# Optimization experiments

Measured on AMD Instinct MI355X. Metric: run time of the kernel, lower is better.

## Reference

```python
import jax, jax.numpy as jnp
import numpy as np

N = 100000   # nodes
E = 800000   # edges
L = 128      # latent_size
S = 15       # message passing steps
TW = 5       # time_window
OUT = 3      # output_size
NT = 3       # node types
NODE_F = 6   # 1+1+1+NT
EDGE_F = 7   # 2+1+2+1+1


def setup_inputs() -> dict:
    key = jax.random.key(0)
    ks = iter(jax.random.split(key, 80))
    def rn(shape, s=1.0):
        return jax.random.normal(next(ks), shape, jnp.float32) * s
    w = 0.05
    d = {}
    d["pvf"] = rn((N, 1))
    d["mat_param_D"] = rn((N, 1))
    d["mat_param_X"] = rn((N, 1))
    d["node_type"] = jax.random.randint(next(ks), (N,), 0, NT)
    d["mesh_pos"] = jax.random.uniform(next(ks), (N, 2), jnp.float32)
    d["world_pos"] = jax.random.uniform(next(ks), (N, 2), jnp.float32)
    d["senders"] = jax.random.randint(next(ks), (E,), 0, N)
    d["receivers"] = jax.random.randint(next(ks), (E,), 0, N)
    # normalizer stats
    d["node_norm_mean"] = rn((NODE_F,), 0.1); d["node_norm_std"] = jnp.ones((NODE_F,), jnp.float32)
    d["edge_norm_mean"] = rn((EDGE_F,), 0.1); d["edge_norm_std"] = jnp.ones((EDGE_F,), jnp.float32)
    # node encoder
    d["ne_w1"] = rn((NODE_F, L), w); d["ne_b1"] = jnp.zeros((L,), jnp.float32)
    d["ne_w2"] = rn((L, L), w);      d["ne_b2"] = jnp.zeros((L,), jnp.float32)
    d["ne_g"] = jnp.ones((L,), jnp.float32); d["ne_be"] = jnp.zeros((L,), jnp.float32)
    # edge encoder
    d["ee_w1"] = rn((EDGE_F, L), w); d["ee_b1"] = jnp.zeros((L,), jnp.float32)
    d["ee_w2"] = rn((L, L), w);      d["ee_b2"] = jnp.zeros((L,), jnp.float32)
    d["ee_g"] = jnp.ones((L,), jnp.float32); d["ee_be"] = jnp.zeros((L,), jnp.float32)
    # stacked GraphNetBlock params (S blocks)
    d["blk_ew1"] = rn((S, 3 * L, L), w); d["blk_eb1"] = jnp.zeros((S, L), jnp.float32)
    d["blk_ew2"] = rn((S, L, L), w);     d["blk_eb2"] = jnp.zeros((S, L), jnp.float32)
    d["blk_eg"] = jnp.ones((S, L), jnp.float32); d["blk_ebt"] = jnp.zeros((S, L), jnp.float32)
    d["blk_nw1"] = rn((S, 2 * L, L), w); d["blk_nb1"] = jnp.zeros((S, L), jnp.float32)
    d["blk_nw2"] = rn((S, L, L), w);     d["blk_nb2"] = jnp.zeros((S, L), jnp.float32)
    d["blk_ng"] = jnp.ones((S, L), jnp.float32); d["blk_nbt"] = jnp.zeros((S, L), jnp.float32)
    # decoder (Conv1d k=1 == per-node Linear)
    d["dec_w1"] = rn((L, 8), w); d["dec_b1"] = jnp.zeros((8,), jnp.float32)
    d["dec_w2"] = rn((8, OUT * TW), w); d["dec_b2"] = jnp.zeros((OUT * TW,), jnp.float32)
    return d


def _mlp_ln(x, w1, b1, w2, b2, g, b):
    # Linear-ReLU-Linear-ReLU-LayerNorm
    h = jax.nn.relu(x @ w1 + b1)
    h = jax.nn.relu(h @ w2 + b2)
    mu = jnp.mean(h, axis=-1, keepdims=True)
    var = jnp.var(h, axis=-1, keepdims=True)
    return (h - mu) * jax.lax.rsqrt(var + 1e-5) * g + b


def _forward(pvf, mat_param_D, mat_param_X, node_type, mesh_pos, world_pos, senders, receivers,
             node_norm_mean, node_norm_std, edge_norm_mean, edge_norm_std,
             ne_w1, ne_b1, ne_w2, ne_b2, ne_g, ne_be,
             ee_w1, ee_b1, ee_w2, ee_b2, ee_g, ee_be,
             blk_ew1, blk_eb1, blk_ew2, blk_eb2, blk_eg, blk_ebt,
             blk_nw1, blk_nb1, blk_nw2, blk_nb2, blk_ng, blk_nbt,
             dec_w1, dec_b1, dec_w2, dec_b2):
    # --- build features ---
    one_hot = jax.nn.one_hot(node_type, NT, dtype=jnp.float32)
    node_feats = jnp.concatenate([pvf, mat_param_D, mat_param_X, one_hot], axis=-1)   # [N, NODE_F]
    rel_m = mesh_pos[senders] - mesh_pos[receivers]
    dist_m = jnp.linalg.norm(rel_m, axis=-1, keepdims=True)
    rel_w = world_pos[senders] - world_pos[receivers]
    dist_w = jnp.linalg.norm(rel_w, axis=-1, keepdims=True)
    pvf_grad = pvf[senders] - pvf[receivers]
    edge_feats = jnp.concatenate([rel_m, dist_m, rel_w, dist_w, pvf_grad], axis=-1)   # [E, EDGE_F]
    # --- encode ---
    nl = _mlp_ln((node_feats - node_norm_mean) / node_norm_std, ne_w1, ne_b1, ne_w2, ne_b2, ne_g, ne_be)
    el = _mlp_ln((edge_feats - edge_norm_mean) / edge_norm_std, ee_w1, ee_b1, ee_w2, ee_b2, ee_g, ee_be)
    # --- process: S GraphNetBlocks with residuals ---
    def step(carry, p):
        nl, el = carry
        ew1, eb1, ew2, eb2, eg, ebt, nw1, nb1, nw2, nb2, ng, nbt = p
        edge_in = jnp.concatenate([nl[senders], nl[receivers], el], axis=-1)          # [E, 3L]
        new_e = _mlp_ln(edge_in, ew1, eb1, ew2, eb2, eg, ebt)
        aggr = jax.ops.segment_sum(new_e, receivers, num_segments=N)                  # [N, L]
        new_n = _mlp_ln(jnp.concatenate([nl, aggr], axis=-1), nw1, nb1, nw2, nb2, ng, nbt)
        return (nl + new_n, el + new_e), None
    (nl, el), _ = jax.lax.scan(step, (nl, el),
                               (blk_ew1, blk_eb1, blk_ew2, blk_eb2, blk_eg, blk_ebt,
                                blk_nw1, blk_nb1, blk_nw2, blk_nb2, blk_ng, blk_nbt))
    # --- decode (Conv1d k=1 == Linear) ---
    h = nl @ dec_w1 + dec_b1
    h = h * jax.nn.sigmoid(h)                                                         # Swish beta=1
    decoded = h @ dec_w2 + dec_b2                                                     # [N, OUT*TW]
    dt = jnp.repeat(jnp.arange(1, TW + 1, dtype=jnp.float32), OUT)                    # repeat_interleave
    delta = (decoded * dt).reshape(N, TW, OUT).transpose(1, 0, 2)                     # [TW, N, OUT]
    return delta


def reference(pvf, mat_param_D, mat_param_X, node_type, mesh_pos, world_pos, senders, receivers,
              node_norm_mean, node_norm_std, edge_norm_mean, edge_norm_std,
              ne_w1, ne_b1, ne_w2, ne_b2, ne_g, ne_be,
              ee_w1, ee_b1, ee_w2, ee_b2, ee_g, ee_be,
              blk_ew1, blk_eb1, blk_ew2, blk_eb2, blk_eg, blk_ebt,
              blk_nw1, blk_nb1, blk_nw2, blk_nb2, blk_ng, blk_nbt,
              dec_w1, dec_b1, dec_w2, dec_b2):
    return _forward(pvf, mat_param_D, mat_param_X, node_type, mesh_pos, world_pos, senders, receivers,
                    node_norm_mean, node_norm_std, edge_norm_mean, edge_norm_std,
                    ne_w1, ne_b1, ne_w2, ne_b2, ne_g, ne_be,
                    ee_w1, ee_b1, ee_w2, ee_b2, ee_g, ee_be,
                    blk_ew1, blk_eb1, blk_ew2, blk_eb2, blk_eg, blk_ebt,
                    blk_nw1, blk_nb1, blk_nw2, blk_nb2, blk_ng, blk_nbt,
                    dec_w1, dec_b1, dec_w2, dec_b2)
```

## Files before the change

kernel.cpp:

```cpp
#include <hip/hip_runtime.h>
#include <math.h>

#define NNODES 100000
#define NEDGES 800000
#define L 128
#define NBSCAN ((NNODES + 255) / 256)

typedef unsigned short u16;
typedef unsigned int u32;
typedef unsigned short ushort8 __attribute__((ext_vector_type(8)));
typedef _Float16 f16x8 __attribute__((ext_vector_type(8)));
typedef __attribute__((ext_vector_type(4))) float f32x4;

static __device__ __forceinline__ float h2f(u16 u) {
    _Float16 h;
    __builtin_memcpy(&h, &u, 2);
    return (float)h;
}
static __device__ __forceinline__ u16 f2h(float x) {
    _Float16 h = (_Float16)x;
    u16 u;
    __builtin_memcpy(&u, &h, 2);
    return u;
}
static __device__ __forceinline__ void load8h(const u16* p, float* d) {
    ushort8 v = *(const ushort8*)p;
    #pragma unroll
    for (int k = 0; k < 8; k++) d[k] = h2f(v[k]);
}
static __device__ __forceinline__ void atomic_pk_add_f16(u16* addr, u32 data) {
    asm volatile("global_atomic_pk_add_f16 %0, %1, off" :: "v"(addr), "v"(data));
}

__global__ __launch_bounds__(256) void zero_kernel(uint4* p, int n) {
    int i = blockIdx.x * 256 + threadIdx.x;
    if (i < n) p[i] = make_uint4(0u, 0u, 0u, 0u);
}

__global__ __launch_bounds__(256) void diag_kernel(float* out, int n, float val) {
    int i = blockIdx.x * 256 + threadIdx.x;
    if (i < n) out[i] = val;
}

__global__ __launch_bounds__(256) void count_kernel(
    const int* __restrict__ receivers, u32* __restrict__ counts)
{
    int e = blockIdx.x * 256 + threadIdx.x;
    if (e < NEDGES) atomicAdd(&counts[receivers[e]], 1u);
}

__global__ __launch_bounds__(256) void scan_block_kernel(
    const u32* __restrict__ counts, u32* __restrict__ offsets,
    u32* __restrict__ partials)
{
    __shared__ u32 sh[256];
    int i = blockIdx.x * 256 + threadIdx.x;
    u32 c = (i < NNODES) ? counts[i] : 0u;
    sh[threadIdx.x] = c;
    __syncthreads();
    #pragma unroll
    for (int d = 1; d < 256; d <<= 1) {
        u32 v = (threadIdx.x >= d) ? sh[threadIdx.x - d] : 0u;
        __syncthreads();
        sh[threadIdx.x] += v;
        __syncthreads();
    }
    if (i < NNODES) offsets[i] = sh[threadIdx.x] - c;
    if (threadIdx.x == 255) partials[blockIdx.x] = sh[255];
}

__global__ __launch_bounds__(512) void scan_partials_kernel(u32* __restrict__ partials)
{
    __shared__ u32 sh[512];
    int x = threadIdx.x;
    u32 c = (x < NBSCAN) ? partials[x] : 0u;
    sh[x] = c;
    __syncthreads();
    #pragma unroll
    for (int d = 1; d < 512; d <<= 1) {
        u32 v = (x >= d) ? sh[x - d] : 0u;
        __syncthreads();
        sh[x] += v;
        __syncthreads();
    }
    if (x < NBSCAN) partials[x] = sh[x] - c;
}

__global__ __launch_bounds__(256) void add_offsets_kernel(
    u32* __restrict__ offsets, const u32* __restrict__ partials,
    u32* __restrict__ cursor)
{
    int i = blockIdx.x * 256 + threadIdx.x;
    if (i < NNODES) {
        u32 v = offsets[i] + partials[blockIdx.x];
        offsets[i] = v;
        cursor[i] = v;
    }
}

__global__ __launch_bounds__(256) void scatter_kernel(
    const int* __restrict__ senders, const int* __restrict__ receivers,
    u32* __restrict__ cursor, int* __restrict__ ssorted, int* __restrict__ rsorted)
{
    int e = blockIdx.x * 256 + threadIdx.x;
    if (e < NEDGES) {
        int r = receivers[e];
        u32 pos = atomicAdd(&cursor[r], 1u);
        ssorted[pos] = senders[e];
        rsorted[pos] = r;
    }
}

__global__ __launch_bounds__(256) void pack_weights_kernel(
    const float* __restrict__ src, u16* __restrict__ dst, int K, int nsteps)
{
    int idx = blockIdx.x * 256 + threadIdx.x;
    int nkk = K >> 5;
    int total = nsteps * 8 * nkk * 64;
    if (idx >= total) return;
    int lane = idx & 63;
    int rest = idx >> 6;
    int kk = rest % nkk; rest /= nkk;
    int nb = rest & 7;
    int s = rest >> 3;
    int c15 = lane & 15, gg = lane >> 4;
    const float* w = src + (size_t)s * K * 128;
    u16 out[8];
    #pragma unroll
    for (int j = 0; j < 8; j++) {
        int k = kk * 32 + gg * 8 + j;
        out[j] = f2h(w[(size_t)k * 128 + nb * 16 + c15]);
    }
    *(ushort8*)(dst + (size_t)idx * 8) = *(ushort8*)out;
}

__global__ __launch_bounds__(256) void pack_ee1_kernel(
    const float* __restrict__ src, u16* __restrict__ dst)
{
    int idx = blockIdx.x * 256 + threadIdx.x;
    if (idx >= 8 * 64) return;
    int lane = idx & 63, nb = idx >> 6;
    int c15 = lane & 15, gg = lane >> 4;
    u16 out[8];
    #pragma unroll
    for (int j = 0; j < 8; j++) {
        int k = gg * 8 + j;
        out[j] = (k < 7) ? f2h(src[(size_t)k * 128 + nb * 16 + c15]) : (u16)0;
    }
    *(ushort8*)(dst + (size_t)idx * 8) = *(ushort8*)out;
}

__global__ __launch_bounds__(256) void node_encode_kernel(
    const float* __restrict__ pvf, const float* __restrict__ matD,
    const float* __restrict__ matX, const int* __restrict__ ntype,
    const float* __restrict__ nmean, const float* __restrict__ nstd,
    const float* __restrict__ w1, const float* __restrict__ b1,
    const float* __restrict__ w2, const float* __restrict__ b2,
    const float* __restrict__ g, const float* __restrict__ be,
    u16* __restrict__ nl)
{
    __shared__ float xs[64][8];
    __shared__ float h[64][132];
    const int t = threadIdx.x;
    const int base = blockIdx.x * 64;
    if (t < 64) {
        int n = base + t;
        if (n < NNODES) {
            int nt = ntype[n];
            float f[6];
            f[0] = pvf[n]; f[1] = matD[n]; f[2] = matX[n];
            f[3] = (nt == 0) ? 1.f : 0.f;
            f[4] = (nt == 1) ? 1.f : 0.f;
            f[5] = (nt == 2) ? 1.f : 0.f;
            #pragma unroll
            for (int k = 0; k < 6; k++) xs[t][k] = (f[k] - nmean[k]) / nstd[k];
        } else {
            #pragma unroll
            for (int k = 0; k < 6; k++) xs[t][k] = 0.f;
        }
    }
    __syncthreads();
    const int j = t & 127, half = t >> 7;
    for (int i = 0; i < 32; i++) {
        int e = half * 32 + i;
        float acc = b1[j];
        #pragma unroll
        for (int k = 0; k < 6; k++) acc += xs[e][k] * w1[k * L + j];
        h[e][j] = fmaxf(acc, 0.f);
    }
    __syncthreads();
    float acc2[32];
    #pragma unroll
    for (int i = 0; i < 32; i++) acc2[i] = b2[j];
    for (int k4 = 0; k4 < 32; k4++) {
        const float* wp = w2 + k4 * 4 * L + j;
        float wa = wp[0], wb = wp[L], wc = wp[2 * L], wd = wp[3 * L];
        #pragma unroll
        for (int i = 0; i < 32; i++) {
            const float4 xv = *(const float4*)&h[half * 32 + i][k4 * 4];
            acc2[i] += xv.x * wa + xv.y * wb + xv.z * wc + xv.w * wd;
        }
    }
    __syncthreads();
    #pragma unroll
    for (int i = 0; i < 32; i++) h[half * 32 + i][j] = fmaxf(acc2[i], 0.f);
    __syncthreads();
    {
        const int e = t >> 2, tg = t & 3;
        float sum = 0.f, sq = 0.f;
        #pragma unroll
        for (int jj = 0; jj < 32; jj++) { float v = h[e][tg * 32 + jj]; sum += v; sq += v * v; }
        sum += __shfl_xor(sum, 1); sq += __shfl_xor(sq, 1);
        sum += __shfl_xor(sum, 2); sq += __shfl_xor(sq, 2);
        float mu = sum * (1.f / 128.f);
        float rstd = rsqrtf(sq * (1.f / 128.f) - mu * mu + 1e-5f);
        int n = base + e;
        if (n < NNODES) {
            u32* nrow = (u32*)(nl + (size_t)n * L) + tg * 16;
            #pragma unroll
            for (int p = 0; p < 16; p++) {
                int f0 = tg * 32 + 2 * p;
                float v0 = (h[e][f0] - mu) * rstd * g[f0] + be[f0];
                float v1 = (h[e][f0 + 1] - mu) * rstd * g[f0 + 1] + be[f0 + 1];
                nrow[p] = (u32)f2h(v0) | ((u32)f2h(v1) << 16);
            }
        }
    }
}

__global__ __launch_bounds__(256, 2) void edge_encode_kernel(
    const int* __restrict__ ssorted, const int* __restrict__ rsorted,
    const float* __restrict__ pvf, const float* __restrict__ mesh,
    const float* __restrict__ world,
    const float* __restrict__ emean, const float* __restrict__ estd,
    const u16* __restrict__ wp1, const float* __restrict__ b1,
    const u16* __restrict__ wp2, const float* __restrict__ b2,
    const float* __restrict__ gamma, const float* __restrict__ beta,
    u16* __restrict__ el)
{
    __shared__ __align__(16) u16 hbuf[4][2][4][64][8];
    const int t = threadIdx.x;
    const int wid = t >> 6, lane = t & 63;
    const int c15 = lane & 15, g = lane >> 4;
    const int base = blockIdx.x * 256 + wid * 64;

    f16x8 a[4];
    #pragma unroll
    for (int m = 0; m < 4; m++) {
        f16x8 v;
        #pragma unroll
        for (int k = 0; k < 8; k++) v[k] = (_Float16)0.f;
        if (g == 0) {
            int e = base + m * 16 + c15;
            int s = ssorted[e], r = rsorted[e];
            float rmx = mesh[s * 2] - mesh[r * 2];
            float rmy = mesh[s * 2 + 1] - mesh[r * 2 + 1];
            float dm = sqrtf(rmx * rmx + rmy * rmy);
            float rwx = world[s * 2] - world[r * 2];
            float rwy = world[s * 2 + 1] - world[r * 2 + 1];
            float dw = sqrtf(rwx * rwx + rwy * rwy);
            float pg = pvf[s] - pvf[r];
            float f[7] = {rmx, rmy, dm, rwx, rwy, dw, pg};
            #pragma unroll
            for (int k = 0; k < 7; k++)
                v[k] = (_Float16)((f[k] - emean[k]) / estd[k]);
        }
        a[m] = v;
    }

    f32x4 acc[8][4];
    #pragma unroll
    for (int nb = 0; nb < 8; nb++) {
        float bv = b1[nb * 16 + c15];
        #pragma unroll
        for (int m = 0; m < 4; m++) acc[nb][m] = (f32x4){bv, bv, bv, bv};
    }
    #pragma unroll
    for (int nb = 0; nb < 8; nb++) {
        f16x8 b = *(const f16x8*)(wp1 + ((size_t)(nb * 64 + lane)) * 8);
        #pragma unroll
        for (int m = 0; m < 4; m++)
            acc[nb][m] = __builtin_amdgcn_mfma_f32_16x16x32_f16(a[m], b, acc[nb][m], 0, 0, 0);
    }

    float gamv[8], btv[8];
    #pragma unroll
    for (int nb = 0; nb < 8; nb++) {
        gamv[nb] = gamma[nb * 16 + c15];
        btv[nb] = beta[nb * 16 + c15];
    }
    #pragma unroll
    for (int mp = 0; mp < 2; mp++) {
        #pragma unroll
        for (int ml = 0; ml < 2; ml++) {
            int m = mp * 2 + ml;
            #pragma unroll
            for (int nb = 0; nb < 8; nb++) {
                int kk2 = nb >> 1;
                int sub = ((nb & 1) << 1) | (c15 >> 3);
                int jj = c15 & 7;
                #pragma unroll
                for (int i = 0; i < 4; i++) {
                    float v = fmaxf(acc[nb][m][i], 0.f);
                    hbuf[wid][ml][kk2][g * 4 + i + 16 * sub][jj] = f2h(v);
                }
            }
        }
        f32x4 acc2[2][8];
        #pragma unroll
        for (int nb = 0; nb < 8; nb++) {
            float bv = b2[nb * 16 + c15];
            acc2[0][nb] = (f32x4){bv, bv, bv, bv};
            acc2[1][nb] = (f32x4){bv, bv, bv, bv};
        }
        #pragma unroll
        for (int kk = 0; kk < 4; kk++) {
            f16x8 a0 = *(const f16x8*)&hbuf[wid][0][kk][lane][0];
            f16x8 a1 = *(const f16x8*)&hbuf[wid][1][kk][lane][0];
            #pragma unroll
            for (int nb = 0; nb < 8; nb++) {
                f16x8 b = *(const f16x8*)(wp2 + ((size_t)(nb * 4 + kk) * 64 + lane) * 8);
                acc2[0][nb] = __builtin_amdgcn_mfma_f32_16x16x32_f16(a0, b, acc2[0][nb], 0, 0, 0);
                acc2[1][nb] = __builtin_amdgcn_mfma_f32_16x16x32_f16(a1, b, acc2[1][nb], 0, 0, 0);
            }
        }
        #pragma unroll
        for (int ml = 0; ml < 2; ml++) {
            float muv[4], rsv[4];
            #pragma unroll
            for (int i = 0; i < 4; i++) {
                float p = 0.f, q = 0.f;
                #pragma unroll
                for (int nb = 0; nb < 8; nb++) {
                    float v = fmaxf(acc2[ml][nb][i], 0.f);
                    acc2[ml][nb][i] = v;
                    p += v; q += v * v;
                }
                p += __shfl_xor(p, 1); q += __shfl_xor(q, 1);
                p += __shfl_xor(p, 2); q += __shfl_xor(q, 2);
                p += __shfl_xor(p, 4); q += __shfl_xor(q, 4);
                p += __shfl_xor(p, 8); q += __shfl_xor(q, 8);
                float mu = p * (1.f / 128.f);
                muv[i] = mu;
                rsv[i] = rsqrtf(q * (1.f / 128.f) - mu * mu + 1e-5f);
            }
            #pragma unroll
            for (int i = 0; i < 4; i++) {
                int erow = base + (mp * 2 + ml) * 16 + g * 4 + i;
                #pragma unroll
                for (int nb = 0; nb < 8; nb++) {
                    float v = (acc2[ml][nb][i] - muv[i]) * rsv[i] * gamv[nb] + btv[nb];
                    float pv = __shfl_xor(v, 1);
                    if (!(c15 & 1)) {
                        *(u32*)(el + (size_t)erow * L + nb * 16 + c15) =
                            (u32)f2h(v) | ((u32)f2h(pv) << 16);
                    }
                }
            }
        }
    }
}

#define EDGE_LOAD_A(nk, slot)                                                     \
    {                                                                             \
        _Pragma("unroll")                                                         \
        for (int m = 0; m < 4; m++) {                                             \
            const u16* ap;                                                        \
            if ((nk) < 4)      ap = nl + (size_t)sA[m] * L + (nk) * 32 + g * 8;   \
            else if ((nk) < 8) ap = nl + (size_t)rA[m] * L + ((nk) - 4) * 32 + g * 8; \
            else               ap = el + (size_t)(base + m * 16 + c15) * L + ((nk) - 8) * 32 + g * 8; \
            ab[slot][m] = *(const f16x8*)ap;                                      \
        }                                                                         \
    }

#define NODE_LOAD_A(nk, slot)                                                     \
    {                                                                             \
        _Pragma("unroll")                                                         \
        for (int m = 0; m < 4; m++) {                                             \
            const u16* ap = ((nk) < 4) ? (nl + (size_t)rowL[m] * L + (nk) * 32 + g * 8) \
                                       : (aggr + (size_t)rowL[m] * L + ((nk) - 4) * 32 + g * 8); \
            ab[slot][m] = *(const f16x8*)ap;                                      \
        }                                                                         \
    }

#define LGKM_BARRIER()                                          \
    asm volatile("s_waitcnt lgkmcnt(0)" ::: "memory");          \
    __builtin_amdgcn_sched_barrier(0);                          \
    __builtin_amdgcn_s_barrier();

__global__ __launch_bounds__(256, 2) void edge_block_kernel(
    const int* __restrict__ ssorted, const int* __restrict__ rsorted,
    const u16* __restrict__ nl, u16* __restrict__ el, u16* __restrict__ aggr,
    const u16* __restrict__ wp1, const float* __restrict__ b1,
    const u16* __restrict__ wp2, const float* __restrict__ b2,
    const float* __restrict__ gamma, const float* __restrict__ beta)
{
    __shared__ __align__(16) u16 wbuf[2][8][64][8];
    __shared__ __align__(16) u16 hbuf[4][2][4][64][8];
    const int t = threadIdx.x;
    const int wid = t >> 6, lane = t & 63;
    const int c15 = lane & 15, g = lane >> 4;
    const int base = blockIdx.x * 256 + wid * 64;

    int sA[4], rA[4];
    #pragma unroll
    for (int m = 0; m < 4; m++) {
        sA[m] = ssorted[base + m * 16 + c15];
        rA[m] = rsorted[base + m * 16 + c15];
    }

    f32x4 acc[8][4];
    #pragma unroll
    for (int nb = 0; nb < 8; nb++) {
        float bv = b1[nb * 16 + c15];
        #pragma unroll
        for (int m = 0; m < 4; m++) acc[nb][m] = (f32x4){bv, bv, bv, bv};
    }
    f16x8 ab[2][4];
    f16x8 w0, w1;
    w0 = *(const f16x8*)(wp1 + ((size_t)((2 * wid) * 12 + 0) * 64 + lane) * 8);
    w1 = *(const f16x8*)(wp1 + ((size_t)((2 * wid + 1) * 12 + 0) * 64 + lane) * 8);
    EDGE_LOAD_A(0, 0);
    *(f16x8*)&wbuf[0][2 * wid][lane][0] = w0;
    *(f16x8*)&wbuf[0][2 * wid + 1][lane][0] = w1;
    LGKM_BARRIER();

    #pragma unroll
    for (int kk = 0; kk < 12; kk++) {
        if (kk < 11) {
            w0 = *(const f16x8*)(wp1 + ((size_t)((2 * wid) * 12 + kk + 1) * 64 + lane) * 8);
            w1 = *(const f16x8*)(wp1 + ((size_t)((2 * wid + 1) * 12 + kk + 1) * 64 + lane) * 8);
            EDGE_LOAD_A(kk + 1, (kk + 1) & 1);
        }
        __builtin_amdgcn_s_setprio(1);
        #pragma unroll
        for (int nb = 0; nb < 8; nb++) {
            f16x8 b = *(const f16x8*)&wbuf[kk & 1][nb][lane][0];
            #pragma unroll
            for (int m = 0; m < 4; m++)
                acc[nb][m] = __builtin_amdgcn_mfma_f32_16x16x32_f16(ab[kk & 1][m], b, acc[nb][m], 0, 0, 0);
        }
        __builtin_amdgcn_s_setprio(0);
        if (kk < 11) {
            *(f16x8*)&wbuf[(kk + 1) & 1][2 * wid][lane][0] = w0;
            *(f16x8*)&wbuf[(kk + 1) & 1][2 * wid + 1][lane][0] = w1;
            LGKM_BARRIER();
        }
    }

    float gamv[8], btv[8];
    #pragma unroll
    for (int nb = 0; nb < 8; nb++) {
        gamv[nb] = gamma[nb * 16 + c15];
        btv[nb] = beta[nb * 16 + c15];
    }
    #pragma unroll
    for (int mp = 0; mp < 2; mp++) {
        #pragma unroll
        for (int ml = 0; ml < 2; ml++) {
            int m = mp * 2 + ml;
            #pragma unroll
            for (int nb = 0; nb < 8; nb++) {
                int kk2 = nb >> 1;
                int sub = ((nb & 1) << 1) | (c15 >> 3);
                int jj = c15 & 7;
                #pragma unroll
                for (int i = 0; i < 4; i++) {
                    float v = fmaxf(acc[nb][m][i], 0.f);
                    hbuf[wid][ml][kk2][g * 4 + i + 16 * sub][jj] = f2h(v);
                }
            }
        }
        f32x4 acc2[2][8];
        #pragma unroll
        for (int nb = 0; nb < 8; nb++) {
            float bv = b2[nb * 16 + c15];
            acc2[0][nb] = (f32x4){bv, bv, bv, bv};
            acc2[1][nb] = (f32x4){bv, bv, bv, bv};
        }
        __builtin_amdgcn_s_setprio(1);
        #pragma unroll
        for (int kk = 0; kk < 4; kk++) {
            f16x8 a0 = *(const f16x8*)&hbuf[wid][0][kk][lane][0];
            f16x8 a1 = *(const f16x8*)&hbuf[wid][1][kk][lane][0];
            #pragma unroll
            for (int nb = 0; nb < 8; nb++) {
                f16x8 b = *(const f16x8*)(wp2 + ((size_t)(nb * 4 + kk) * 64 + lane) * 8);
                acc2[0][nb] = __builtin_amdgcn_mfma_f32_16x16x32_f16(a0, b, acc2[0][nb], 0, 0, 0);
                acc2[1][nb] = __builtin_amdgcn_mfma_f32_16x16x32_f16(a1, b, acc2[1][nb], 0, 0, 0);
            }
        }
        __builtin_amdgcn_s_setprio(0);
        #pragma unroll
        for (int ml = 0; ml < 2; ml++) {
            const int slot = mp * 2 + ml;
            float muv[4], rsv[4];
            #pragma unroll
            for (int i = 0; i < 4; i++) {
                float p = 0.f, q = 0.f;
                #pragma unroll
                for (int nb = 0; nb < 8; nb++) {
                    float v = fmaxf(acc2[ml][nb][i], 0.f);
                    acc2[ml][nb][i] = v;
                    p += v; q += v * v;
                }
                p += __shfl_xor(p, 1); q += __shfl_xor(q, 1);
                p += __shfl_xor(p, 2); q += __shfl_xor(q, 2);
                p += __shfl_xor(p, 4); q += __shfl_xor(q, 4);
                p += __shfl_xor(p, 8); q += __shfl_xor(q, 8);
                float mu = p * (1.f / 128.f);
                muv[i] = mu;
                rsv[i] = rsqrtf(q * (1.f / 128.f) - mu * mu + 1e-5f);
            }
            float av[8], apv[8];
            #pragma unroll
            for (int nb = 0; nb < 8; nb++) { av[nb] = 0.f; apv[nb] = 0.f; }
            int cur = rsorted[base + slot * 16 + g * 4];
            #pragma unroll
            for (int i = 0; i < 4; i++) {
                int erow = base + slot * 16 + g * 4 + i;
                int ri = (i == 0) ? cur : rsorted[erow];
                float vv[8], pp[8];
                #pragma unroll
                for (int nb = 0; nb < 8; nb++) {
                    float v = (acc2[ml][nb][i] - muv[i]) * rsv[i] * gamv[nb] + btv[nb];
                    vv[nb] = v;
                    pp[nb] = __shfl_xor(v, 1);
                }
                u32 olds[8];
                if (!(c15 & 1)) {
                    #pragma unroll
                    for (int nb = 0; nb < 8; nb++)
                        olds[nb] = *(const u32*)(el + (size_t)erow * L + nb * 16 + c15);
                }
                if (ri != cur) {
                    #pragma unroll
                    for (int nb = 0; nb < 8; nb++) {
                        if (!(c15 & 1)) {
                            u32 add = (u32)f2h(av[nb]) | ((u32)f2h(apv[nb]) << 16);
                            atomic_pk_add_f16(aggr + (size_t)cur * L + nb * 16 + c15, add);
                        }
                        av[nb] = 0.f; apv[nb] = 0.f;
                    }
                    cur = ri;
                }
                #pragma unroll
                for (int nb = 0; nb < 8; nb++) {
                    av[nb] += vv[nb];
                    apv[nb] += pp[nb];
                    if (!(c15 & 1)) {
                        float r0 = h2f((u16)(olds[nb] & 0xFFFFu)) + vv[nb];
                        float r1 = h2f((u16)(olds[nb] >> 16)) + pp[nb];
                        *(u32*)(el + (size_t)erow * L + nb * 16 + c15) =
                            (u32)f2h(r0) | ((u32)f2h(r1) << 16);
                    }
                }
            }
            #pragma unroll
            for (int nb = 0; nb < 8; nb++) {
                if (!(c15 & 1)) {
                    u32 add = (u32)f2h(av[nb]) | ((u32)f2h(apv[nb]) << 16);
                    atomic_pk_add_f16(aggr + (size_t)cur * L + nb * 16 + c15, add);
                }
            }
        }
    }
}

__global__ __launch_bounds__(256, 2) void node_block_kernel(
    u16* __restrict__ nl, u16* __restrict__ aggr,
    const u16* __restrict__ wp1, const float* __restrict__ b1,
    const u16* __restrict__ wp2, const float* __restrict__ b2,
    const float* __restrict__ gamma, const float* __restrict__ beta)
{
    __shared__ __align__(16) u16 wbuf[2][8][64][8];
    __shared__ __align__(16) u16 hbuf[4][2][4][64][8];
    const int t = threadIdx.x;
    const int wid = t >> 6, lane = t & 63;
    const int c15 = lane & 15, g = lane >> 4;
    const int base = blockIdx.x * 256 + wid * 64;

    int rowL[4];
    #pragma unroll
    for (int m = 0; m < 4; m++) {
        int r = base + m * 16 + c15;
        rowL[m] = r < NNODES ? r : 0;
    }

    f32x4 acc[8][4];
    #pragma unroll
    for (int nb = 0; nb < 8; nb++) {
        float bv = b1[nb * 16 + c15];
        #pragma unroll
        for (int m = 0; m < 4; m++) acc[nb][m] = (f32x4){bv, bv, bv, bv};
    }
    f16x8 ab[2][4];
    f16x8 w0, w1;
    w0 = *(const f16x8*)(wp1 + ((size_t)((2 * wid) * 8 + 0) * 64 + lane) * 8);
    w1 = *(const f16x8*)(wp1 + ((size_t)((2 * wid + 1) * 8 + 0) * 64 + lane) * 8);
    NODE_LOAD_A(0, 0);
    *(f16x8*)&wbuf[0][2 * wid][lane][0] = w0;
    *(f16x8*)&wbuf[0][2 * wid + 1][lane][0] = w1;
    LGKM_BARRIER();

    #pragma unroll
    for (int kk = 0; kk < 8; kk++) {
        if (kk < 7) {
            w0 = *(const f16x8*)(wp1 + ((size_t)((2 * wid) * 8 + kk + 1) * 64 + lane) * 8);
            w1 = *(const f16x8*)(wp1 + ((size_t)((2 * wid + 1) * 8 + kk + 1) * 64 + lane) * 8);
            NODE_LOAD_A(kk + 1, (kk + 1) & 1);
        }
        __builtin_amdgcn_s_setprio(1);
        #pragma unroll
        for (int nb = 0; nb < 8; nb++) {
            f16x8 b = *(const f16x8*)&wbuf[kk & 1][nb][lane][0];
            #pragma unroll
            for (int m = 0; m < 4; m++)
                acc[nb][m] = __builtin_amdgcn_mfma_f32_16x16x32_f16(ab[kk & 1][m], b, acc[nb][m], 0, 0, 0);
        }
        __builtin_amdgcn_s_setprio(0);
        if (kk < 7) {
            *(f16x8*)&wbuf[(kk + 1) & 1][2 * wid][lane][0] = w0;
            *(f16x8*)&wbuf[(kk + 1) & 1][2 * wid + 1][lane][0] = w1;
            LGKM_BARRIER();
        }
    }

    {
        const uint4 z4 = make_uint4(0u, 0u, 0u, 0u);
        #pragma unroll
        for (int m = 0; m < 4; m++) {
            int r = base + m * 16 + c15;
            if (r < NNODES) {
                #pragma unroll
                for (int kk = 0; kk < 4; kk++)
                    *(uint4*)(aggr + (size_t)r * L + kk * 32 + g * 8) = z4;
            }
        }
    }

    float gamv[8], btv[8];
    #pragma unroll
    for (int nb = 0; nb < 8; nb++) {
        gamv[nb] = gamma[nb * 16 + c15];
        btv[nb] = beta[nb * 16 + c15];
    }
    #pragma unroll
    for (int mp = 0; mp < 2; mp++) {
        #pragma unroll
        for (int ml = 0; ml < 2; ml++) {
            int m = mp * 2 + ml;
            #pragma unroll
            for (int nb = 0; nb < 8; nb++) {
                int kk2 = nb >> 1;
                int sub = ((nb & 1) << 1) | (c15 >> 3);
                int jj = c15 & 7;
                #pragma unroll
                for (int i = 0; i < 4; i++) {
                    float v = fmaxf(acc[nb][m][i], 0.f);
                    hbuf[wid][ml][kk2][g * 4 + i + 16 * sub][jj] = f2h(v);
                }
            }
        }
        f32x4 acc2[2][8];
        #pragma unroll
        for (int nb = 0; nb < 8; nb++) {
            float bv = b2[nb * 16 + c15];
            acc2[0][nb] = (f32x4){bv, bv, bv, bv};
            acc2[1][nb] = (f32x4){bv, bv, bv, bv};
        }
        __builtin_amdgcn_s_setprio(1);
        #pragma unroll
        for (int kk = 0; kk < 4; kk++) {
            f16x8 a0 = *(const f16x8*)&hbuf[wid][0][kk][lane][0];
            f16x8 a1 = *(const f16x8*)&hbuf[wid][1][kk][lane][0];
            #pragma unroll
            for (int nb = 0; nb < 8; nb++) {
                f16x8 b = *(const f16x8*)(wp2 + ((size_t)(nb * 4 + kk) * 64 + lane) * 8);
                acc2[0][nb] = __builtin_amdgcn_mfma_f32_16x16x32_f16(a0, b, acc2[0][nb], 0, 0, 0);
                acc2[1][nb] = __builtin_amdgcn_mfma_f32_16x16x32_f16(a1, b, acc2[1][nb], 0, 0, 0);
            }
        }
        __builtin_amdgcn_s_setprio(0);
        #pragma unroll
        for (int ml = 0; ml < 2; ml++) {
            float muv[4], rsv[4];
            #pragma unroll
            for (int i = 0; i < 4; i++) {
                float p = 0.f, q = 0.f;
                #pragma unroll
                for (int nb = 0; nb < 8; nb++) {
                    float v = fmaxf(acc2[ml][nb][i], 0.f);
                    acc2[ml][nb][i] = v;
                    p += v; q += v * v;
                }
                p += __shfl_xor(p, 1); q += __shfl_xor(q, 1);
                p += __shfl_xor(p, 2); q += __shfl_xor(q, 2);
                p += __shfl_xor(p, 4); q += __shfl_xor(q, 4);
                p += __shfl_xor(p, 8); q += __shfl_xor(q, 8);
                float mu = p * (1.f / 128.f);
                muv[i] = mu;
                rsv[i] = rsqrtf(q * (1.f / 128.f) - mu * mu + 1e-5f);
            }
            #pragma unroll
            for (int i = 0; i < 4; i++) {
                int nrow = base + (mp * 2 + ml) * 16 + g * 4 + i;
                #pragma unroll
                for (int nb = 0; nb < 8; nb++) {
                    float v = (acc2[ml][nb][i] - muv[i]) * rsv[i] * gamv[nb] + btv[nb];
                    float pv = __shfl_xor(v, 1);
                    if (!(c15 & 1) && nrow < NNODES) {
                        int col = nb * 16 + c15;
                        u32* nlp = (u32*)(nl + (size_t)nrow * L + col);
                        u32 old = *nlp;
                        float r0 = h2f((u16)(old & 0xFFFFu)) + v;
                        float r1 = h2f((u16)(old >> 16)) + pv;
                        *nlp = (u32)f2h(r0) | ((u32)f2h(r1) << 16);
                    }
                }
            }
        }
    }
}

__global__ __launch_bounds__(256) void decode_kernel(
    const u16* __restrict__ nl,
    const float* __restrict__ w1, const float* __restrict__ b1,
    const float* __restrict__ w2, const float* __restrict__ b2,
    float* __restrict__ out)
{
    int n = blockIdx.x * blockDim.x + threadIdx.x;
    if (n >= NNODES) return;
    float h8[8];
    #pragma unroll
    for (int jj = 0; jj < 8; jj++) h8[jj] = b1[jj];
    const u16* row = nl + (size_t)n * L;
    for (int k = 0; k < L; k += 8) {
        float xv[8];
        load8h(row + k, xv);
        #pragma unroll
        for (int q = 0; q < 8; q++)
            #pragma unroll
            for (int jj = 0; jj < 8; jj++)
                h8[jj] += xv[q] * w1[(k + q) * 8 + jj];
    }
    #pragma unroll
    for (int jj = 0; jj < 8; jj++) { float v = h8[jj]; h8[jj] = v / (1.f + expf(-v)); }
    #pragma unroll
    for (int o15 = 0; o15 < 15; o15++) {
        float accv = b2[o15];
        #pragma unroll
        for (int jj = 0; jj < 8; jj++) accv += h8[jj] * w2[jj * 15 + o15];
        int tt = o15 / 3, oo = o15 - tt * 3;
        out[(size_t)tt * NNODES * 3 + (size_t)n * 3 + oo] = accv * (float)(tt + 1);
    }
}

extern "C" void kernel_launch(void* const* d_in, const int* in_sizes, int n_in,
                              void* d_out, int out_size, void* d_ws, size_t ws_size,
                              hipStream_t stream)
{
    const size_t AG_B = (size_t)NNODES * L * 2;
    const size_t EL_B = (size_t)NEDGES * L * 2;
    const size_t NL_B = (size_t)NNODES * L * 2;
    const size_t PE1_N = (size_t)15 * 8 * 12 * 64 * 8;
    const size_t PE2_N = (size_t)15 * 8 * 4 * 64 * 8;
    const size_t PN1_N = (size_t)15 * 8 * 8 * 64 * 8;
    const size_t PN2_N = (size_t)15 * 8 * 4 * 64 * 8;
    const size_t PEE1_N = (size_t)8 * 64 * 8;
    const size_t PEE2_N = (size_t)8 * 4 * 64 * 8;
    const size_t WPK_B = (PE1_N + PE2_N + PN1_N + PN2_N + PEE1_N + PEE2_N) * 2;
    const size_t SS_B  = (size_t)NEDGES * 4;
    const size_t RS_B  = (size_t)NEDGES * 4;
    const size_t CNT_B = (size_t)NNODES * 4;
    const size_t OFF_B = (size_t)NNODES * 4;
    const size_t CUR_B = (size_t)NNODES * 4;
    const size_t PAR_B = 2048;
    const size_t TOTAL = AG_B + EL_B + NL_B + WPK_B + SS_B + RS_B
                       + CNT_B + OFF_B + CUR_B + PAR_B;

    if (ws_size < TOTAL) {
        float val = 1000.0f + (float)((double)ws_size * 1e-6);
        diag_kernel<<<(out_size + 255) / 256, 256, 0, stream>>>((float*)d_out, out_size, val);
        return;
    }

    char* wsp = (char*)d_ws;
    u16* aggr = (u16*)wsp;                 wsp += AG_B;
    u16* el   = (u16*)wsp;                 wsp += EL_B;
    u16* nl   = (u16*)wsp;                 wsp += NL_B;
    u16* pe1  = (u16*)wsp;                 wsp += PE1_N * 2;
    u16* pe2  = (u16*)wsp;                 wsp += PE2_N * 2;
    u16* pn1  = (u16*)wsp;                 wsp += PN1_N * 2;
    u16* pn2  = (u16*)wsp;                 wsp += PN2_N * 2;
    u16* pee1 = (u16*)wsp;                 wsp += PEE1_N * 2;
    u16* pee2 = (u16*)wsp;                 wsp += PEE2_N * 2;
    int* ssorted = (int*)wsp;              wsp += SS_B;
    int* rsorted = (int*)wsp;              wsp += RS_B;
    u32* counts  = (u32*)wsp;              wsp += CNT_B;
    u32* offsets = (u32*)wsp;              wsp += OFF_B;
    u32* cursor  = (u32*)wsp;              wsp += CUR_B;
    u32* partials = (u32*)wsp;             wsp += PAR_B;
    float* out = (float*)d_out;

    const float* pvf       = (const float*)d_in[0];
    const float* matD      = (const float*)d_in[1];
    const float* matX      = (const float*)d_in[2];
    const int*   ntype     = (const int*)d_in[3];
    const float* mesh      = (const float*)d_in[4];
    const float* world     = (const float*)d_in[5];
    const int*   senders   = (const int*)d_in[6];
    const int*   receivers = (const int*)d_in[7];
    const float* nmean = (const float*)d_in[8];
    const float* nstd  = (const float*)d_in[9];
    const float* emean = (const float*)d_in[10];
    const float* estd  = (const float*)d_in[11];
    const float* ne_w1 = (const float*)d_in[12];
    const float* ne_b1 = (const float*)d_in[13];
    const float* ne_w2 = (const float*)d_in[14];
    const float* ne_b2 = (const float*)d_in[15];
    const float* ne_g  = (const float*)d_in[16];
    const float* ne_be = (const float*)d_in[17];
    const float* ee_w1 = (const float*)d_in[18];
    const float* ee_b1 = (const float*)d_in[19];
    const float* ee_w2 = (const float*)d_in[20];
    const float* ee_b2 = (const float*)d_in[21];
    const float* ee_g  = (const float*)d_in[22];
    const float* ee_be = (const float*)d_in[23];
    const float* blk_ew1 = (const float*)d_in[24];
    const float* blk_eb1 = (const float*)d_in[25];
    const float* blk_ew2 = (const float*)d_in[26];
    const float* blk_eb2 = (const float*)d_in[27];
    const float* blk_eg  = (const float*)d_in[28];
    const float* blk_ebt = (const float*)d_in[29];
    const float* blk_nw1 = (const float*)d_in[30];
    const float* blk_nb1 = (const float*)d_in[31];
    const float* blk_nw2 = (const float*)d_in[32];
    const float* blk_nb2 = (const float*)d_in[33];
    const float* blk_ng  = (const float*)d_in[34];
    const float* blk_nbt = (const float*)d_in[35];
    const float* dec_w1 = (const float*)d_in[36];
    const float* dec_b1 = (const float*)d_in[37];
    const float* dec_w2 = (const float*)d_in[38];
    const float* dec_b2 = (const float*)d_in[39];

    zero_kernel<<<(int)((CNT_B / 16 + 255) / 256), 256, 0, stream>>>((uint4*)counts, (int)(CNT_B / 16));
    count_kernel<<<(NEDGES + 255) / 256, 256, 0, stream>>>(receivers, counts);
    scan_block_kernel<<<NBSCAN, 256, 0, stream>>>(counts, offsets, partials);
    scan_partials_kernel<<<1, 512, 0, stream>>>(partials);
    add_offsets_kernel<<<NBSCAN, 256, 0, stream>>>(offsets, partials, cursor);
    scatter_kernel<<<(NEDGES + 255) / 256, 256, 0, stream>>>(senders, receivers, cursor, ssorted, rsorted);

    pack_weights_kernel<<<(int)((15 * 8 * 12 * 64 + 255) / 256), 256, 0, stream>>>(
        blk_ew1, pe1, 384, 15);
    pack_weights_kernel<<<(int)((15 * 8 * 4 * 64 + 255) / 256), 256, 0, stream>>>(
        blk_ew2, pe2, 128, 15);
    pack_weights_kernel<<<(int)((15 * 8 * 8 * 64 + 255) / 256), 256, 0, stream>>>(
        blk_nw1, pn1, 256, 15);
    pack_weights_kernel<<<(int)((15 * 8 * 4 * 64 + 255) / 256), 256, 0, stream>>>(
        blk_nw2, pn2, 128, 15);
    pack_ee1_kernel<<<2, 256, 0, stream>>>(ee_w1, pee1);
    pack_weights_kernel<<<(int)((8 * 4 * 64 + 255) / 256), 256, 0, stream>>>(
        ee_w2, pee2, 128, 1);

    node_encode_kernel<<<(NNODES + 63) / 64, 256, 0, stream>>>(
        pvf, matD, matX, ntype, nmean, nstd,
        ne_w1, ne_b1, ne_w2, ne_b2, ne_g, ne_be, nl);
    edge_encode_kernel<<<NEDGES / 256, 256, 0, stream>>>(
        ssorted, rsorted, pvf, mesh, world, emean, estd,
        pee1, ee_b1, pee2, ee_b2, ee_g, ee_be, el);

    const int nzero = NNODES * L * 2 / 16;
    zero_kernel<<<(nzero + 255) / 256, 256, 0, stream>>>((uint4*)aggr, nzero);

    for (int s = 0; s < 15; s++) {
        edge_block_kernel<<<NEDGES / 256, 256, 0, stream>>>(
            ssorted, rsorted, nl, el, aggr,
            pe1 + (size_t)s * 8 * 12 * 64 * 8, blk_eb1 + s * L,
            pe2 + (size_t)s * 8 * 4 * 64 * 8,  blk_eb2 + s * L,
            blk_eg + s * L, blk_ebt + s * L);
        node_block_kernel<<<(NNODES + 255) / 256, 256, 0, stream>>>(
            nl, aggr,
            pn1 + (size_t)s * 8 * 8 * 64 * 8, blk_nb1 + s * L,
            pn2 + (size_t)s * 8 * 4 * 64 * 8, blk_nb2 + s * L,
            blk_ng + s * L, blk_nbt + s * L);
    }

    decode_kernel<<<(NNODES + 255) / 256, 256, 0, stream>>>(
        nl, dec_w1, dec_b1, dec_w2, dec_b2, out);
}
```

Before: 6.844 ms.

## Use single-wave blocks with per-wave register weight prefetch instead of shared LDS tiles

```diff
diff --git a/kernel.cpp b/kernel.cpp
--- a/kernel.cpp
+++ b/kernel.cpp
@@ -383,24 +383,21 @@
         }                                                                         \
     }
 
-#define LGKM_BARRIER()                                          \
+#define WAVE_LDS_FENCE()                                        \
     asm volatile("s_waitcnt lgkmcnt(0)" ::: "memory");          \
-    __builtin_amdgcn_sched_barrier(0);                          \
-    __builtin_amdgcn_s_barrier();
-
-__global__ __launch_bounds__(256, 2) void edge_block_kernel(
+    __builtin_amdgcn_sched_barrier(0);
+
+__global__ __launch_bounds__(64, 2) void edge_block_kernel(
     const int* __restrict__ ssorted, const int* __restrict__ rsorted,
     const u16* __restrict__ nl, u16* __restrict__ el, u16* __restrict__ aggr,
     const u16* __restrict__ wp1, const float* __restrict__ b1,
     const u16* __restrict__ wp2, const float* __restrict__ b2,
     const float* __restrict__ gamma, const float* __restrict__ beta)
 {
-    __shared__ __align__(16) u16 wbuf[2][8][64][8];
-    __shared__ __align__(16) u16 hbuf[4][2][4][64][8];
-    const int t = threadIdx.x;
-    const int wid = t >> 6, lane = t & 63;
+    __shared__ __align__(16) u16 hbuf[2][4][64][8];
+    const int lane = threadIdx.x & 63;
     const int c15 = lane & 15, g = lane >> 4;
-    const int base = blockIdx.x * 256 + wid * 64;
+    const int base = blockIdx.x * 64;
 
     int sA[4], rA[4];
     #pragma unroll
@@ -417,35 +414,30 @@
         for (int m = 0; m < 4; m++) acc[nb][m] = (f32x4){bv, bv, bv, bv};
     }
     f16x8 ab[2][4];
-    f16x8 w0, w1;
-    w0 = *(const f16x8*)(wp1 + ((size_t)((2 * wid) * 12 + 0) * 64 + lane) * 8);
-    w1 = *(const f16x8*)(wp1 + ((size_t)((2 * wid + 1) * 12 + 0) * 64 + lane) * 8);
+    f16x8 bbuf[2][8];
+    #pragma unroll
+    for (int nb = 0; nb < 8; nb++)
+        bbuf[0][nb] = *(const f16x8*)(wp1 + ((size_t)(nb * 12) * 64 + lane) * 8);
     EDGE_LOAD_A(0, 0);
-    *(f16x8*)&wbuf[0][2 * wid][lane][0] = w0;
-    *(f16x8*)&wbuf[0][2 * wid + 1][lane][0] = w1;
-    LGKM_BARRIER();
 
     #pragma unroll
     for (int kk = 0; kk < 12; kk++) {
         if (kk < 11) {
-            w0 = *(const f16x8*)(wp1 + ((size_t)((2 * wid) * 12 + kk + 1) * 64 + lane) * 8);
-            w1 = *(const f16x8*)(wp1 + ((size_t)((2 * wid + 1) * 12 + kk + 1) * 64 + lane) * 8);
+            #pragma unroll
+            for (int nb = 0; nb < 8; nb++)
+                bbuf[(kk + 1) & 1][nb] =
+                    *(const f16x8*)(wp1 + ((size_t)(nb * 12 + kk + 1) * 64 + lane) * 8);
             EDGE_LOAD_A(kk + 1, (kk + 1) & 1);
         }
         __builtin_amdgcn_s_setprio(1);
         #pragma unroll
         for (int nb = 0; nb < 8; nb++) {
-            f16x8 b = *(const f16x8*)&wbuf[kk & 1][nb][lane][0];
             #pragma unroll
             for (int m = 0; m < 4; m++)
-                acc[nb][m] = __builtin_amdgcn_mfma_f32_16x16x32_f16(ab[kk & 1][m], b, acc[nb][m], 0, 0, 0);
+                acc[nb][m] = __builtin_amdgcn_mfma_f32_16x16x32_f16(
+                    ab[kk & 1][m], bbuf[kk & 1][nb], acc[nb][m], 0, 0, 0);
         }
         __builtin_amdgcn_s_setprio(0);
-        if (kk < 11) {
-            *(f16x8*)&wbuf[(kk + 1) & 1][2 * wid][lane][0] = w0;
-            *(f16x8*)&wbuf[(kk + 1) & 1][2 * wid + 1][lane][0] = w1;
-            LGKM_BARRIER();
-        }
     }
 
     float gamv[8], btv[8];
@@ -467,10 +459,11 @@
                 #pragma unroll
                 for (int i = 0; i < 4; i++) {
                     float v = fmaxf(acc[nb][m][i], 0.f);
-                    hbuf[wid][ml][kk2][g * 4 + i + 16 * sub][jj] = f2h(v);
-                }
-            }
-        }
+                    hbuf[ml][kk2][g * 4 + i + 16 * sub][jj] = f2h(v);
+                }
+            }
+        }
+        WAVE_LDS_FENCE();
         f32x4 acc2[2][8];
         #pragma unroll
         for (int nb = 0; nb < 8; nb++) {
@@ -481,8 +474,8 @@
         __builtin_amdgcn_s_setprio(1);
         #pragma unroll
         for (int kk = 0; kk < 4; kk++) {
-            f16x8 a0 = *(const f16x8*)&hbuf[wid][0][kk][lane][0];
-            f16x8 a1 = *(const f16x8*)&hbuf[wid][1][kk][lane][0];
+            f16x8 a0 = *(const f16x8*)&hbuf[0][kk][lane][0];
+            f16x8 a1 = *(const f16x8*)&hbuf[1][kk][lane][0];
             #pragma unroll
             for (int nb = 0; nb < 8; nb++) {
                 f16x8 b = *(const f16x8*)(wp2 + ((size_t)(nb * 4 + kk) * 64 + lane) * 8);
@@ -491,6 +484,7 @@
             }
         }
         __builtin_amdgcn_s_setprio(0);
+        WAVE_LDS_FENCE();
         #pragma unroll
         for (int ml = 0; ml < 2; ml++) {
             const int slot = mp * 2 + ml;
@@ -567,18 +561,16 @@
     }
 }
 
-__global__ __launch_bounds__(256, 2) void node_block_kernel(
+__global__ __launch_bounds__(64, 2) void node_block_kernel(
     u16* __restrict__ nl, u16* __restrict__ aggr,
     const u16* __restrict__ wp1, const float* __restrict__ b1,
     const u16* __restrict__ wp2, const float* __restrict__ b2,
     const float* __restrict__ gamma, const float* __restrict__ beta)
 {
-    __shared__ __align__(16) u16 wbuf[2][8][64][8];
-    __shared__ __align__(16) u16 hbuf[4][2][4][64][8];
-    const int t = threadIdx.x;
-    const int wid = t >> 6, lane = t & 63;
+    __shared__ __align__(16) u16 hbuf[2][4][64][8];
+    const int lane = threadIdx.x & 63;
     const int c15 = lane & 15, g = lane >> 4;
-    const int base = blockIdx.x * 256 + wid * 64;
+    const int base = blockIdx.x * 64;
 
     int rowL[4];
     #pragma unroll
@@ -595,35 +587,30 @@
         for (int m = 0; m < 4; m++) acc[nb][m] = (f32x4){bv, bv, bv, bv};
     }
     f16x8 ab[2][4];
-    f16x8 w0, w1;
-    w0 = *(const f16x8*)(wp1 + ((size_t)((2 * wid) * 8 + 0) * 64 + lane) * 8);
-    w1 = *(const f16x8*)(wp1 + ((size_t)((2 * wid + 1) * 8 + 0) * 64 + lane) * 8);
+    f16x8 bbuf[2][8];
+    #pragma unroll
+    for (int nb = 0; nb < 8; nb++)
+        bbuf[0][nb] = *(const f16x8*)(wp1 + ((size_t)(nb * 8) * 64 + lane) * 8);
     NODE_LOAD_A(0, 0);
-    *(f16x8*)&wbuf[0][2 * wid][lane][0] = w0;
-    *(f16x8*)&wbuf[0][2 * wid + 1][lane][0] = w1;
-    LGKM_BARRIER();
 
     #pragma unroll
     for (int kk = 0; kk < 8; kk++) {
         if (kk < 7) {
-            w0 = *(const f16x8*)(wp1 + ((size_t)((2 * wid) * 8 + kk + 1) * 64 + lane) * 8);
-            w1 = *(const f16x8*)(wp1 + ((size_t)((2 * wid + 1) * 8 + kk + 1) * 64 + lane) * 8);
+            #pragma unroll
+            for (int nb = 0; nb < 8; nb++)
+                bbuf[(kk + 1) & 1][nb] =
+                    *(const f16x8*)(wp1 + ((size_t)(nb * 8 + kk + 1) * 64 + lane) * 8);
             NODE_LOAD_A(kk + 1, (kk + 1) & 1);
         }
         __builtin_amdgcn_s_setprio(1);
         #pragma unroll
         for (int nb = 0; nb < 8; nb++) {
-            f16x8 b = *(const f16x8*)&wbuf[kk & 1][nb][lane][0];
             #pragma unroll
             for (int m = 0; m < 4; m++)
-                acc[nb][m] = __builtin_amdgcn_mfma_f32_16x16x32_f16(ab[kk & 1][m], b, acc[nb][m], 0, 0, 0);
+                acc[nb][m] = __builtin_amdgcn_mfma_f32_16x16x32_f16(
+                    ab[kk & 1][m], bbuf[kk & 1][nb], acc[nb][m], 0, 0, 0);
         }
         __builtin_amdgcn_s_setprio(0);
-        if (kk < 7) {
-            *(f16x8*)&wbuf[(kk + 1) & 1][2 * wid][lane][0] = w0;
-            *(f16x8*)&wbuf[(kk + 1) & 1][2 * wid + 1][lane][0] = w1;
-            LGKM_BARRIER();
-        }
     }
 
     {
@@ -658,10 +645,11 @@
                 #pragma unroll
                 for (int i = 0; i < 4; i++) {
                     float v = fmaxf(acc[nb][m][i], 0.f);
-                    hbuf[wid][ml][kk2][g * 4 + i + 16 * sub][jj] = f2h(v);
-                }
-            }
-        }
+                    hbuf[ml][kk2][g * 4 + i + 16 * sub][jj] = f2h(v);
+                }
+            }
+        }
+        WAVE_LDS_FENCE();
         f32x4 acc2[2][8];
         #pragma unroll
         for (int nb = 0; nb < 8; nb++) {
@@ -672,8 +660,8 @@
         __builtin_amdgcn_s_setprio(1);
         #pragma unroll
         for (int kk = 0; kk < 4; kk++) {
-            f16x8 a0 = *(const f16x8*)&hbuf[wid][0][kk][lane][0];
-            f16x8 a1 = *(const f16x8*)&hbuf[wid][1][kk][lane][0];
+            f16x8 a0 = *(const f16x8*)&hbuf[0][kk][lane][0];
+            f16x8 a1 = *(const f16x8*)&hbuf[1][kk][lane][0];
             #pragma unroll
             for (int nb = 0; nb < 8; nb++) {
                 f16x8 b = *(const f16x8*)(wp2 + ((size_t)(nb * 4 + kk) * 64 + lane) * 8);
@@ -682,6 +670,7 @@
             }
         }
         __builtin_amdgcn_s_setprio(0);
+        WAVE_LDS_FENCE();
         #pragma unroll
         for (int ml = 0; ml < 2; ml++) {
             float muv[4], rsv[4];
@@ -874,12 +863,12 @@
     zero_kernel<<<(nzero + 255) / 256, 256, 0, stream>>>((uint4*)aggr, nzero);
 
     for (int s = 0; s < 15; s++) {
-        edge_block_kernel<<<NEDGES / 256, 256, 0, stream>>>(
+        edge_block_kernel<<<NEDGES / 64, 64, 0, stream>>>(
             ssorted, rsorted, nl, el, aggr,
             pe1 + (size_t)s * 8 * 12 * 64 * 8, blk_eb1 + s * L,
             pe2 + (size_t)s * 8 * 4 * 64 * 8,  blk_eb2 + s * L,
             blk_eg + s * L, blk_ebt + s * L);
-        node_block_kernel<<<(NNODES + 255) / 256, 256, 0, stream>>>(
+        node_block_kernel<<<(NNODES + 63) / 64, 64, 0, stream>>>(
             nl, aggr,
             pn1 + (size_t)s * 8 * 8 * 64 * 8, blk_nb1 + s * L,
             pn2 + (size_t)s * 8 * 4 * 64 * 8, blk_nb2 + s * L,
```

New measurement: 8.109 ms. 1.18x slower.
